# Optimization experiments

Measured on AMD Instinct MI355X. Metric: run time of the kernel, lower is better.

The kernel has to match this reference:

```python
import jax, jax.numpy as jnp
import numpy as np

B, T = 2048, 256
VOCAB, E, H = 50000, 50, 50


def setup_inputs() -> dict:
    key = jax.random.key(0)
    ks = jax.random.split(key, 9)
    s = 0.1
    return {
        "batched_input": jax.random.randint(ks[0], (B, T), 0, VOCAB),
        "emb": jax.random.normal(ks[1], (VOCAB, E)) * s,
        "Wk": jax.random.normal(ks[2], (E, 4 * H)) * s,      # LSTM input kernel (i,f,c,o)
        "Uk": jax.random.normal(ks[3], (H, 4 * H)) * s,      # LSTM recurrent kernel
        "b": jnp.zeros((4 * H,)),                            # LSTM bias
        "W1": jax.random.normal(ks[4], (H, E)) * s,          # denseTypeOne (applied twice)
        "b1": jnp.zeros((E,)),
        "W2": jax.random.normal(ks[5], (E, 1)) * s,          # denseTypeTwo
        "b2": jnp.zeros((1,)),
    }


def _lstm(xg, Uk):
    # xg: [T, B, 4H] precomputed input projections; Keras gate order i,f,c,o
    Bsz = xg.shape[1]
    h0 = jnp.zeros((Bsz, H), xg.dtype)
    c0 = jnp.zeros((Bsz, H), xg.dtype)

    def step(carry, xt):
        h, c = carry
        z = xt + h @ Uk
        i, f, g, o = jnp.split(z, 4, axis=-1)
        i = jax.nn.sigmoid(i)
        f = jax.nn.sigmoid(f)
        g = jnp.tanh(g)
        o = jax.nn.sigmoid(o)
        c = f * c + i * g
        h = o * jnp.tanh(c)
        return (h, c), h

    (_, _), hs = jax.lax.scan(step, (h0, c0), xg)
    return hs  # [T, B, H]


def reference(batched_input, emb, Wk, Uk, b, W1, b1, W2, b2):
    x = emb[batched_input]                                  # [B, T, E]
    xg = jnp.einsum('bte,eg->tbg', x, Wk) + b               # [T, B, 4H]
    hs = _lstm(xg, Uk)                                      # [T, B, H]
    hs = jnp.transpose(hs, (1, 0, 2))                       # [B, T, H]
    d1 = jax.nn.relu(hs @ W1 + b1)                          # denseTypeOne
    d2 = jax.nn.relu(d1 @ W1 + b1)                          # denseTypeOne again (as in source)
    p = jax.nn.sigmoid(d2 @ W2 + b2)                        # [B, T, 1]
    return p.reshape(p.shape[0], -1)                        # Flatten -> [B, T]
```

## Files before the change

kernel.cpp:

```cpp
#include <hip/hip_runtime.h>


typedef unsigned short u16;
typedef unsigned int   u32;
typedef float f32x4 __attribute__((ext_vector_type(4)));
typedef short s16x8 __attribute__((ext_vector_type(8)));

__device__ __forceinline__ float bf2f(u16 u){
  union { u32 i; float f; } v; v.i = ((u32)u) << 16; return v.f;
}
__device__ __forceinline__ u16 f2bf(float f){
  union { float fl; u32 i; } v; v.fl = f;
  u32 r = v.i + 0x7fffu + ((v.i >> 16) & 1u);
  return (u16)(r >> 16);
}
__device__ __forceinline__ float frcp(float x){ return __builtin_amdgcn_rcpf(x); }
__device__ __forceinline__ float sigm_f(float x){
  float e = __expf(-x);
  return frcp(1.f + e);
}
__device__ __forceinline__ float tanh_f(float x){
  x = fminf(fmaxf(x, -15.f), 15.f);
  float e = __expf(-2.f * x);
  return (1.f - e) * frcp(1.f + e);
}
__device__ __forceinline__ f32x4 mf(s16x8 a, s16x8 b, f32x4 c){
  return __builtin_amdgcn_mfma_f32_16x16x32_bf16(a, b, c, 0, 0, 0);
}
__device__ __forceinline__ float ldf(const void* p, int i, bool f32in){
  if (f32in) return ((const float*)p)[i];
  return bf2f(((const u16*)p)[i]);
}

#define TPB 256
#define RPB 8

extern "C" __global__ __launch_bounds__(TPB, 1) void LSTM_Seq2Dis_15272903704706_kernel(
    const int* idx, const void* emb, const void* Wk, const void* Uk,
    const void* bias, const void* W1, const void* b1,
    const void* W2, const void* b2, float* out)
{
  __shared__ __align__(16) u16 ering[2][16][1024];
  __shared__ __align__(16) u16 abuf[2][1024];
  __shared__ __align__(16) u16 hbuf[8][2][512];
  __shared__ __align__(16) u16 dwork[4][2][512];
  __shared__ int   tokl[2048];
  __shared__ int   s_f32;

  const int tid = threadIdx.x;
  const int wv  = tid >> 6, ln = tid & 63;
  const int r0  = blockIdx.x * RPB;

  if (tid == 0){
    const u32* ew = (const u32*)emb;
    int hits = 0;
    for (int i = 0; i < 64; i++){
      u32 ef = (ew[i] >> 7) & 0xFFu;
      if (ef >= 112u && ef <= 127u) hits++;
    }
    s_f32 = (hits < 32) ? 1 : 0;
  }

  for (int i = tid; i < 2*16*1024; i += TPB) ((u16*)ering)[i] = 0;
  for (int i = tid; i < 2*1024;   i += TPB) ((u16*)abuf)[i]  = 0;
  for (int i = tid; i < 8*2*512;  i += TPB) ((u16*)hbuf)[i]  = 0;
  for (int i = tid; i < 2048;     i += TPB){
    int r = i & 7, s = i >> 3;
    tokl[i] = idx[(r0 + r)*256 + s];
  }
  __syncthreads();
  const bool f32in = (s_f32 != 0);

  const int jown = wv*16 + (ln & 15);
  const bool jval = (jown < 50);
  s16x8 bz[4][4];
  #pragma unroll
  for (int t = 0; t < 4; t++){
    const int col = t*50 + jown;
    #pragma unroll
    for (int kt = 0; kt < 4; kt++){
      s16x8 v;
      #pragma unroll
      for (int j = 0; j < 8; j++){
        int k = kt*32 + ((ln >> 4) << 3) + j;
        float w = 0.f;
        if (jval){
          if (k < 50)                  w = ldf(Uk, k*200 + col, f32in);
          else if (k >= 64 && k < 114) w = ldf(Wk, (k-64)*200 + col, f32in);
        }
        v[j] = (short)f2bf(w);
      }
      bz[t][kt] = v;
    }
  }
  float bg[4];
  #pragma unroll
  for (int t = 0; t < 4; t++)
    bg[t] = jval ? ldf(bias, t*50 + jown, f32in) : 0.f;

  s16x8 w1f[4][2];
  float b1v[4], w2v[4];
  #pragma unroll
  for (int nt = 0; nt < 4; nt++){
    int c = nt*16 + (ln & 15);
    b1v[nt] = (c < 50) ? ldf(b1, c, f32in) : 0.f;
    w2v[nt] = (c < 50) ? ldf(W2, c, f32in) : 0.f;
    #pragma unroll
    for (int kt = 0; kt < 2; kt++){
      s16x8 v;
      #pragma unroll
      for (int j = 0; j < 8; j++){
        int k = kt*32 + ((ln >> 4) << 3) + j;
        v[j] = (short)((k < 50 && c < 50) ? f2bf(ldf(W1, k*50 + c, f32in)) : (u16)0);
      }
      w1f[nt][kt] = v;
    }
  }
  const float b2s = ldf(b2, 0, f32in);

  const int gr = tid / 50, gj = tid - gr*50;
  const int foff = (gj >> 5)*512 + (gr + (((gj & 31) >> 3) << 4))*8 + (gj & 7);

  const int q  = ln >> 4;
  const int hi = q >> 1;
  const int rowbase = (q & 1)*4 + hi*2;
  float creg[2] = {0.f, 0.f};
  const int eo16 = ((jown & 31) >> 3) << 4;
  const int aoff0 = (jown >> 5)*512 + (rowbase + eo16)*8 + (jown & 7);

  auto dense_head = [&](int tcd){
    #pragma unroll
    for (int p = 0; p < 2; p++){
      const int mt = 2*wv + p;
      s16x8 a0 = *(const s16x8*)&hbuf[mt][0][ln*8];
      s16x8 a1 = *(const s16x8*)&hbuf[mt][1][ln*8];
      #pragma unroll
      for (int nt = 0; nt < 4; nt++){
        f32x4 acc = {0.f,0.f,0.f,0.f};
        acc = mf(a0, w1f[nt][0], acc);
        acc = mf(a1, w1f[nt][1], acc);
        int c = nt*16 + (ln & 15);
        #pragma unroll
        for (int r = 0; r < 4; r++){
          float v = fmaxf(acc[r] + b1v[nt], 0.f);
          int row16 = ((ln >> 4) << 2) + r;
          dwork[wv][c >> 5][(row16 + (((c & 31) >> 3) << 4))*8 + (c & 7)] = f2bf(v);
        }
      }
      s16x8 d0 = *(const s16x8*)&dwork[wv][0][ln*8];
      s16x8 d1 = *(const s16x8*)&dwork[wv][1][ln*8];
      float part[4] = {0.f,0.f,0.f,0.f};
      #pragma unroll
      for (int nt = 0; nt < 4; nt++){
        f32x4 acc = {0.f,0.f,0.f,0.f};
        acc = mf(d0, w1f[nt][0], acc);
        acc = mf(d1, w1f[nt][1], acc);
        #pragma unroll
        for (int r = 0; r < 4; r++)
          part[r] += fmaxf(acc[r] + b1v[nt], 0.f) * w2v[nt];
      }
      #pragma unroll
      for (int d = 1; d < 16; d <<= 1)
        #pragma unroll
        for (int r = 0; r < 4; r++) part[r] += __shfl_xor(part[r], d, 16);
      if ((ln & 15) == 0){
        int qq = ln >> 4;
        #pragma unroll
        for (int r = 0; r < 4; r++){
          int m = mt*16 + (qq << 2) + r;
          int sl8 = m >> 3, rb = m & 7;
          float z = part[r] + b2s;
          z = fmaxf(fminf(z, 1.0f), -1.0f);
          out[(r0 + rb)*256 + tcd + sl8] = sigm_f(z);
        }
      }
    }
  };

  float ev[32];
  if (tid < 200){
    #pragma unroll
    for (int sl = 0; sl < 16; sl++){
      ev[sl]      = ldf(emb, tokl[sl*8 + gr]*50 + gj, f32in);
      ev[16 + sl] = ldf(emb, tokl[sl*8 + gr + 4]*50 + gj, f32in);
    }
  }

  for (int ch = 0; ch < 16; ch++){
    const int tc = ch*16;
    const int eb = ch & 1;

    if (tid < 200){
      #pragma unroll
      for (int sl = 0; sl < 16; sl++)
        ering[eb][sl][foff]      = f2bf(ev[sl]);
      #pragma unroll
      for (int sl = 0; sl < 16; sl++)
        ering[eb][sl][foff + 32] = f2bf(ev[16 + sl]);
      if (ch < 15){
        const int tn = tc + 16;
        #pragma unroll
        for (int sl = 0; sl < 16; sl++){
          ev[sl]      = ldf(emb, tokl[(tn + sl)*8 + gr]*50 + gj, f32in);
          ev[16 + sl] = ldf(emb, tokl[(tn + sl)*8 + gr + 4]*50 + gj, f32in);
        }
      }
    }
    if (ch > 0) dense_head(tc - 16);
    __syncthreads();

    s16x8 e0 = *(const s16x8*)&ering[eb][0][ln*8];
    s16x8 e1 = *(const s16x8*)&ering[eb][0][512 + ln*8];
    f32x4 ae[4];
    #pragma unroll
    for (int t = 0; t < 4; t++){
      f32x4 a = {0.f,0.f,0.f,0.f};
      a = mf(e0, bz[t][2], a);
      a = mf(e1, bz[t][3], a);
      ae[t] = a;
    }

    for (int sl = 0; sl < 16; sl++){
      const int s   = tc + sl;
      const int cur = s & 1, nxt = cur ^ 1;

      s16x8 av0 = *(const s16x8*)&abuf[cur][ln*8];
      s16x8 av1 = *(const s16x8*)&abuf[cur][512 + ln*8];
      f32x4 g4[4];
      #pragma unroll
      for (int t = 0; t < 4; t++){
        f32x4 a = {0.f,0.f,0.f,0.f};
        a = mf(av0, bz[t][0], a);
        a = mf(av1, bz[t][1], a);
        g4[t] = a + ae[t];
      }

      float zz[4][2];
      #pragma unroll
      for (int t = 0; t < 4; t++){
        float s2 = __shfl_xor(g4[t][2], 32);
        float s3 = __shfl_xor(g4[t][3], 32);
        zz[t][0] = hi ? s2 : g4[t][0];
        zz[t][1] = hi ? s3 : g4[t][1];
      }

      u16 hb[2];
      #pragma unroll
      for (int rp = 0; rp < 2; rp++){
        float iv = sigm_f(zz[0][rp] + bg[0]);
        float fv = sigm_f(zz[1][rp] + bg[1]);
        float gv = tanh_f(zz[2][rp] + bg[2]);
        float ov = sigm_f(zz[3][rp] + bg[3]);
        float c  = fv * creg[rp] + iv * gv;
        creg[rp] = c;
        hb[rp] = f2bf(ov * tanh_f(c));
      }
      if (jval){
        #pragma unroll
        for (int rp = 0; rp < 2; rp++){
          abuf[nxt][aoff0 + rp*8] = hb[rp];
          int m = sl*8 + rowbase + rp;
          hbuf[m >> 4][jown >> 5][((m & 15) + eo16)*8 + (jown & 7)] = hb[rp];
        }
      }

      if (sl < 15){
        e0 = *(const s16x8*)&ering[eb][sl + 1][ln*8];
        e1 = *(const s16x8*)&ering[eb][sl + 1][512 + ln*8];
        #pragma unroll
        for (int t = 0; t < 4; t++){
          f32x4 a = {0.f,0.f,0.f,0.f};
          a = mf(e0, bz[t][2], a);
          a = mf(e1, bz[t][3], a);
          ae[t] = a;
        }
      }
      __syncthreads();
    }
  }

  dense_head(240);
}

extern "C" void kernel_launch(void* const* d_in, const int* in_sizes, int n_in,
                              void* d_out, int out_size, void* d_ws, size_t ws_size,
                              hipStream_t stream) {
  (void)in_sizes; (void)n_in; (void)out_size; (void)d_ws; (void)ws_size;
  hipLaunchKernelGGL(LSTM_Seq2Dis_15272903704706_kernel,
                     dim3(256), dim3(TPB), 0, stream,
                     (const int*)d_in[0], d_in[1], d_in[2], d_in[3], d_in[4],
                     d_in[5], d_in[6], d_in[7], d_in[8], (float*)d_out);
}
```

Baseline: 305.8 us.

## Halve rows per block and run two LSTM blocks per CU

Cuts the batch rows handled per block from 8 to 4 and doubles the grid to 512 blocks, with launch bounds allowing two blocks per CU. Each lane now computes gates for a single row, using an extra lane shuffle to pick its cell value, and the dense head processes one 16-row tile per wave. The embedding ring is single-buffered to shrink shared memory so two blocks fit per CU. The goal is to hide the latency of the serial recurrence by interleaving two independent blocks on each CU, at the cost of fewer MFMA rows used per step and more sync overhead per row.

```diff
diff --git a/kernel.cpp b/kernel.cpp
--- a/kernel.cpp
+++ b/kernel.cpp
@@ -33,18 +33,18 @@
 }
 
 #define TPB 256
-#define RPB 8
-
-extern "C" __global__ __launch_bounds__(TPB, 1) void LSTM_Seq2Dis_15272903704706_kernel(
+#define RPB 4
+
+extern "C" __global__ __launch_bounds__(TPB, 2) void LSTM_Seq2Dis_15272903704706_kernel(
     const int* idx, const void* emb, const void* Wk, const void* Uk,
     const void* bias, const void* W1, const void* b1,
     const void* W2, const void* b2, float* out)
 {
-  __shared__ __align__(16) u16 ering[2][16][1024];
+  __shared__ __align__(16) u16 ering[16][1024];
   __shared__ __align__(16) u16 abuf[2][1024];
-  __shared__ __align__(16) u16 hbuf[8][2][512];
+  __shared__ __align__(16) u16 hbuf[4][2][512];
   __shared__ __align__(16) u16 dwork[4][2][512];
-  __shared__ int   tokl[2048];
+  __shared__ int   tokl[1024];
   __shared__ int   s_f32;
 
   const int tid = threadIdx.x;
@@ -61,11 +61,11 @@
     s_f32 = (hits < 32) ? 1 : 0;
   }
 
-  for (int i = tid; i < 2*16*1024; i += TPB) ((u16*)ering)[i] = 0;
-  for (int i = tid; i < 2*1024;   i += TPB) ((u16*)abuf)[i]  = 0;
-  for (int i = tid; i < 8*2*512;  i += TPB) ((u16*)hbuf)[i]  = 0;
-  for (int i = tid; i < 2048;     i += TPB){
-    int r = i & 7, s = i >> 3;
+  for (int i = tid; i < 16*1024; i += TPB) ((u16*)ering)[i] = 0;
+  for (int i = tid; i < 2*1024;  i += TPB) ((u16*)abuf)[i]  = 0;
+  for (int i = tid; i < 4*2*512; i += TPB) ((u16*)hbuf)[i]  = 0;
+  for (int i = tid; i < 1024;    i += TPB){
+    int r = i & 3, s = i >> 2;
     tokl[i] = idx[(r0 + r)*256 + s];
   }
   __syncthreads();
@@ -123,94 +123,82 @@
 
   const int q  = ln >> 4;
   const int hi = q >> 1;
-  const int rowbase = (q & 1)*4 + hi*2;
-  float creg[2] = {0.f, 0.f};
+  float creg = 0.f;
   const int eo16 = ((jown & 31) >> 3) << 4;
-  const int aoff0 = (jown >> 5)*512 + (rowbase + eo16)*8 + (jown & 7);
+  const int aoff = (jown >> 5)*512 + (q + eo16)*8 + (jown & 7);
 
   auto dense_head = [&](int tcd){
-    #pragma unroll
-    for (int p = 0; p < 2; p++){
-      const int mt = 2*wv + p;
-      s16x8 a0 = *(const s16x8*)&hbuf[mt][0][ln*8];
-      s16x8 a1 = *(const s16x8*)&hbuf[mt][1][ln*8];
-      #pragma unroll
-      for (int nt = 0; nt < 4; nt++){
-        f32x4 acc = {0.f,0.f,0.f,0.f};
-        acc = mf(a0, w1f[nt][0], acc);
-        acc = mf(a1, w1f[nt][1], acc);
-        int c = nt*16 + (ln & 15);
-        #pragma unroll
-        for (int r = 0; r < 4; r++){
-          float v = fmaxf(acc[r] + b1v[nt], 0.f);
-          int row16 = ((ln >> 4) << 2) + r;
-          dwork[wv][c >> 5][(row16 + (((c & 31) >> 3) << 4))*8 + (c & 7)] = f2bf(v);
-        }
-      }
-      s16x8 d0 = *(const s16x8*)&dwork[wv][0][ln*8];
-      s16x8 d1 = *(const s16x8*)&dwork[wv][1][ln*8];
-      float part[4] = {0.f,0.f,0.f,0.f};
-      #pragma unroll
-      for (int nt = 0; nt < 4; nt++){
-        f32x4 acc = {0.f,0.f,0.f,0.f};
-        acc = mf(d0, w1f[nt][0], acc);
-        acc = mf(d1, w1f[nt][1], acc);
-        #pragma unroll
-        for (int r = 0; r < 4; r++)
-          part[r] += fmaxf(acc[r] + b1v[nt], 0.f) * w2v[nt];
-      }
-      #pragma unroll
-      for (int d = 1; d < 16; d <<= 1)
-        #pragma unroll
-        for (int r = 0; r < 4; r++) part[r] += __shfl_xor(part[r], d, 16);
-      if ((ln & 15) == 0){
-        int qq = ln >> 4;
-        #pragma unroll
-        for (int r = 0; r < 4; r++){
-          int m = mt*16 + (qq << 2) + r;
-          int sl8 = m >> 3, rb = m & 7;
-          float z = part[r] + b2s;
-          z = fmaxf(fminf(z, 1.0f), -1.0f);
-          out[(r0 + rb)*256 + tcd + sl8] = sigm_f(z);
-        }
+    const int mt = wv;
+    s16x8 a0 = *(const s16x8*)&hbuf[mt][0][ln*8];
+    s16x8 a1 = *(const s16x8*)&hbuf[mt][1][ln*8];
+    #pragma unroll
+    for (int nt = 0; nt < 4; nt++){
+      f32x4 acc = {0.f,0.f,0.f,0.f};
+      acc = mf(a0, w1f[nt][0], acc);
+      acc = mf(a1, w1f[nt][1], acc);
+      int c = nt*16 + (ln & 15);
+      #pragma unroll
+      for (int r = 0; r < 4; r++){
+        float v = fmaxf(acc[r] + b1v[nt], 0.f);
+        int row16 = ((ln >> 4) << 2) + r;
+        dwork[wv][c >> 5][(row16 + (((c & 31) >> 3) << 4))*8 + (c & 7)] = f2bf(v);
+      }
+    }
+    s16x8 d0 = *(const s16x8*)&dwork[wv][0][ln*8];
+    s16x8 d1 = *(const s16x8*)&dwork[wv][1][ln*8];
+    float part[4] = {0.f,0.f,0.f,0.f};
+    #pragma unroll
+    for (int nt = 0; nt < 4; nt++){
+      f32x4 acc = {0.f,0.f,0.f,0.f};
+      acc = mf(d0, w1f[nt][0], acc);
+      acc = mf(d1, w1f[nt][1], acc);
+      #pragma unroll
+      for (int r = 0; r < 4; r++)
+        part[r] += fmaxf(acc[r] + b1v[nt], 0.f) * w2v[nt];
+    }
+    #pragma unroll
+    for (int d = 1; d < 16; d <<= 1)
+      #pragma unroll
+      for (int r = 0; r < 4; r++) part[r] += __shfl_xor(part[r], d, 16);
+    if ((ln & 15) == 0){
+      int qq = ln >> 4;
+      #pragma unroll
+      for (int r = 0; r < 4; r++){
+        int m = mt*16 + (qq << 2) + r;
+        int sl4 = m >> 2, rb = m & 3;
+        float z = part[r] + b2s;
+        z = fmaxf(fminf(z, 1.0f), -1.0f);
+        out[(r0 + rb)*256 + tcd + sl4] = sigm_f(z);
       }
     }
   };
 
-  float ev[32];
+  float ev[16];
   if (tid < 200){
     #pragma unroll
-    for (int sl = 0; sl < 16; sl++){
-      ev[sl]      = ldf(emb, tokl[sl*8 + gr]*50 + gj, f32in);
-      ev[16 + sl] = ldf(emb, tokl[sl*8 + gr + 4]*50 + gj, f32in);
-    }
+    for (int sl = 0; sl < 16; sl++)
+      ev[sl] = ldf(emb, tokl[sl*4 + gr]*50 + gj, f32in);
   }
 
   for (int ch = 0; ch < 16; ch++){
     const int tc = ch*16;
-    const int eb = ch & 1;
 
     if (tid < 200){
       #pragma unroll
       for (int sl = 0; sl < 16; sl++)
-        ering[eb][sl][foff]      = f2bf(ev[sl]);
-      #pragma unroll
-      for (int sl = 0; sl < 16; sl++)
-        ering[eb][sl][foff + 32] = f2bf(ev[16 + sl]);
+        ering[sl][foff] = f2bf(ev[sl]);
       if (ch < 15){
         const int tn = tc + 16;
         #pragma unroll
-        for (int sl = 0; sl < 16; sl++){
-          ev[sl]      = ldf(emb, tokl[(tn + sl)*8 + gr]*50 + gj, f32in);
-          ev[16 + sl] = ldf(emb, tokl[(tn + sl)*8 + gr + 4]*50 + gj, f32in);
-        }
+        for (int sl = 0; sl < 16; sl++)
+          ev[sl] = ldf(emb, tokl[(tn + sl)*4 + gr]*50 + gj, f32in);
       }
     }
     if (ch > 0) dense_head(tc - 16);
     __syncthreads();
 
-    s16x8 e0 = *(const s16x8*)&ering[eb][0][ln*8];
-    s16x8 e1 = *(const s16x8*)&ering[eb][0][512 + ln*8];
+    s16x8 e0 = *(const s16x8*)&ering[0][ln*8];
+    s16x8 e1 = *(const s16x8*)&ering[0][512 + ln*8];
     f32x4 ae[4];
     #pragma unroll
     for (int t = 0; t < 4; t++){
@@ -235,38 +223,33 @@
         g4[t] = a + ae[t];
       }
 
-      float zz[4][2];
+      float cell[4];
       #pragma unroll
       for (int t = 0; t < 4; t++){
-        float s2 = __shfl_xor(g4[t][2], 32);
-        float s3 = __shfl_xor(g4[t][3], 32);
-        zz[t][0] = hi ? s2 : g4[t][0];
-        zz[t][1] = hi ? s3 : g4[t][1];
-      }
-
-      u16 hb[2];
-      #pragma unroll
-      for (int rp = 0; rp < 2; rp++){
-        float iv = sigm_f(zz[0][rp] + bg[0]);
-        float fv = sigm_f(zz[1][rp] + bg[1]);
-        float gv = tanh_f(zz[2][rp] + bg[2]);
-        float ov = sigm_f(zz[3][rp] + bg[3]);
-        float c  = fv * creg[rp] + iv * gv;
-        creg[rp] = c;
-        hb[rp] = f2bf(ov * tanh_f(c));
-      }
+        float s2  = __shfl_xor(g4[t][2], 32);
+        float s3  = __shfl_xor(g4[t][3], 32);
+        float zz0 = hi ? s2 : g4[t][0];
+        float zz1 = hi ? s3 : g4[t][1];
+        float w   = __shfl_xor(zz1, 16);
+        cell[t]   = (q & 1) ? w : zz0;
+      }
+
+      float iv = sigm_f(cell[0] + bg[0]);
+      float fv = sigm_f(cell[1] + bg[1]);
+      float gv = tanh_f(cell[2] + bg[2]);
+      float ov = sigm_f(cell[3] + bg[3]);
+      float c  = fv * creg + iv * gv;
+      creg = c;
+      u16 hb = f2bf(ov * tanh_f(c));
       if (jval){
-        #pragma unroll
-        for (int rp = 0; rp < 2; rp++){
-          abuf[nxt][aoff0 + rp*8] = hb[rp];
-          int m = sl*8 + rowbase + rp;
-          hbuf[m >> 4][jown >> 5][((m & 15) + eo16)*8 + (jown & 7)] = hb[rp];
-        }
+        abuf[nxt][aoff] = hb;
+        int m = sl*4 + q;
+        hbuf[m >> 4][jown >> 5][((m & 15) + eo16)*8 + (jown & 7)] = hb;
       }
 
       if (sl < 15){
-        e0 = *(const s16x8*)&ering[eb][sl + 1][ln*8];
-        e1 = *(const s16x8*)&ering[eb][sl + 1][512 + ln*8];
+        e0 = *(const s16x8*)&ering[sl + 1][ln*8];
+        e1 = *(const s16x8*)&ering[sl + 1][512 + ln*8];
         #pragma unroll
         for (int t = 0; t < 4; t++){
           f32x4 a = {0.f,0.f,0.f,0.f};
@@ -287,7 +270,7 @@
                               hipStream_t stream) {
   (void)in_sizes; (void)n_in; (void)out_size; (void)d_ws; (void)ws_size;
   hipLaunchKernelGGL(LSTM_Seq2Dis_15272903704706_kernel,
-                     dim3(256), dim3(TPB), 0, stream,
+                     dim3(512), dim3(TPB), 0, stream,
                      (const int*)d_in[0], d_in[1], d_in[2], d_in[3], d_in[4],
                      d_in[5], d_in[6], d_in[7], d_in[8], (float*)d_out);
 }
```

After: 293.2 us. -4.1%, faster.
